# Performance work log

Measured on AMD Instinct MI355X. Metric: run time of the kernel, lower is better.

The kernel has to match this reference:

```python
import jax, jax.numpy as jnp
import numpy as np

B, S, D, H = 4, 2048, 256, 8
DH = D // H  # d_head = 32


def setup_inputs() -> dict:
    key = jax.random.key(0)
    ks = jax.random.split(key, 7)
    scale = 1.0 / np.sqrt(D)  # ~ torch Linear init range
    sequences = jax.random.normal(ks[0], (B, S, D), dtype=jnp.float32)
    Wq = jax.random.uniform(ks[1], (H, D, DH), jnp.float32, -scale, scale)
    Wk = jax.random.uniform(ks[2], (H, D, DH), jnp.float32, -scale, scale)
    Wv = jax.random.uniform(ks[3], (H, D, DH), jnp.float32, -scale, scale)
    bq = jax.random.uniform(ks[4], (H, DH), jnp.float32, -scale, scale)
    bk = jax.random.uniform(ks[5], (H, DH), jnp.float32, -scale, scale)
    bv = jax.random.uniform(ks[6], (H, DH), jnp.float32, -scale, scale)
    return {"sequences": sequences, "Wq": Wq, "Wk": Wk, "Wv": Wv,
            "bq": bq, "bk": bk, "bv": bv}


def reference(sequences, Wq, Wk, Wv, bq, bk, bv):
    # Per-head linear maps of the FULL token (use_linear_mapping=True):
    # q[b,h,s,e] = sequences[b,s,:] @ Wq[h] + bq[h]
    q = jnp.einsum('bsd,hde->bhse', sequences, Wq) + bq[None, :, None, :]
    k = jnp.einsum('bsd,hde->bhse', sequences, Wk) + bk[None, :, None, :]
    v = jnp.einsum('bsd,hde->bhse', sequences, Wv) + bv[None, :, None, :]
    # Scaled dot-product attention per batch/head (full SxS matrix, as original)
    scores = jnp.einsum('bhse,bhte->bhst', q, k) / jnp.sqrt(jnp.float32(DH))
    attn = jax.nn.softmax(scores, axis=-1)
    out = jnp.einsum('bhst,bhte->bhse', attn, v)
    # hstack heads along feature dim -> [B, S, D]
    return out.transpose(0, 2, 1, 3).reshape(B, S, D)
```

## Files before the change

### kernel.cpp

```cpp
#include <hip/hip_runtime.h>
#include <hip/hip_bf16.h>


#define NB 4
#define NS 2048
#define ND 256
#define NH 8
#define NDH 32
#define KT 128
#define NT (NS / KT)

typedef __attribute__((ext_vector_type(8))) short short8;
typedef __attribute__((ext_vector_type(4))) float float4v;

static __device__ __forceinline__ unsigned short f2bf(float f) {
    union { float f; unsigned int u; } v; v.f = f;
    unsigned int r = (v.u + 0x7FFFu + ((v.u >> 16) & 1u)) >> 16;
    return (unsigned short)r;
}

static __device__ __forceinline__ unsigned int pk2bf(float lo, float hi) {
    __hip_bfloat162 h = __float22bfloat162_rn(float2{lo, hi});
    union { __hip_bfloat162 h; unsigned int u; } c; c.h = h;
    return c.u;
}

#if defined(__has_builtin)
#if __has_builtin(__builtin_amdgcn_exp2f)
#define EXP2F(x) __builtin_amdgcn_exp2f(x)
#endif
#endif
#ifndef EXP2F
#define EXP2F(x) exp2f(x)
#endif

#define SWZ(x) ((x) ^ ((((x) >> 7) & 7) << 4))

__global__ __launch_bounds__(256) void prep_seq(const float* __restrict__ seq,
                                                unsigned short* __restrict__ seqb) {
    int i = (blockIdx.x * 256 + threadIdx.x) * 4;
    float4 v = *(const float4*)(seq + i);
    ushort4 o;
    o.x = f2bf(v.x); o.y = f2bf(v.y); o.z = f2bf(v.z); o.w = f2bf(v.w);
    *(ushort4*)(seqb + i) = o;
}

__global__ __launch_bounds__(256) void prep_w(const float* __restrict__ Wq,
                                              const float* __restrict__ Wk,
                                              const float* __restrict__ Wv,
                                              unsigned short* __restrict__ Wt) {
    int idx = blockIdx.x * 256 + threadIdx.x;
    int c = idx >> 8, d = idx & 255;
    int mat = c >> 8;
    int cm = c & 255;
    int h = cm >> 5, e = cm & 31;
    const float* W = (mat == 0) ? Wq : (mat == 1) ? Wk : Wv;
    Wt[c * 256 + d] = f2bf(W[(h * 256 + d) * 32 + e]);
}

__global__ __launch_bounds__(256, 2) void proj(const unsigned short* __restrict__ seqb,
                                               const unsigned short* __restrict__ Wt,
                                               const float* __restrict__ bq,
                                               const float* __restrict__ bk,
                                               const float* __restrict__ bv,
                                               unsigned short* __restrict__ Q,
                                               unsigned short* __restrict__ K,
                                               unsigned short* __restrict__ Vt) {
    __shared__ __align__(16) unsigned short plds[32768];

    int m0 = blockIdx.x * 64;
    int c0 = blockIdx.y * 64;
    int tid = (int)threadIdx.x;
    int wave = tid >> 6, lane = tid & 63;
    int g = lane >> 4, r4 = lane & 15;

#pragma unroll
    for (int j = 0; j < 16; ++j) {
        int s = tid + 256 * j;
        int local = s & 2047;
        int row = local >> 5;
        int col16 = (local & 31) ^ (row & 7);
        const unsigned short* src = (s < 2048)
            ? (seqb + (size_t)(m0 + row) * 256 + col16 * 8)
            : (Wt + (size_t)(c0 + row) * 256 + col16 * 8);
        __builtin_amdgcn_global_load_lds(
            (const __attribute__((address_space(1))) unsigned int*)src,
            (__attribute__((address_space(3))) unsigned int*)(&plds[s * 8]), 16, 0, 0);
    }
    __syncthreads();

    const unsigned short* ldsA = plds;
    const unsigned short* ldsB = plds + 16384;
    int rowA = wave * 16 + r4;
    int xA = r4 & 7;

    float4v acc[4];
#pragma unroll
    for (int ct = 0; ct < 4; ++ct) acc[ct] = (float4v){0.f, 0.f, 0.f, 0.f};

#pragma unroll
    for (int i = 0; i < 8; ++i) {
        int cp = ((4 * i + g) ^ xA) * 8;
        short8 a = *(const short8*)(ldsA + rowA * 256 + cp);
#pragma unroll
        for (int ct = 0; ct < 4; ++ct) {
            short8 b = *(const short8*)(ldsB + (ct * 16 + r4) * 256 + cp);
            acc[ct] = __builtin_amdgcn_mfma_f32_16x16x32_bf16(a, b, acc[ct], 0, 0, 0);
        }
    }

    const float SC = 0.17677669529663687f * 1.4426950408889634f;
#pragma unroll
    for (int ct = 0; ct < 4; ++ct) {
        int c = c0 + ct * 16 + r4;
        int mat = c >> 8;
        int cm = c & 255;
        int h = cm >> 5, e = cm & 31;
        float bias = ((mat == 0) ? bq : (mat == 1) ? bk : bv)[cm];
#pragma unroll
        for (int r = 0; r < 4; ++r) {
            int m = m0 + wave * 16 + 4 * g + r;
            int b = m >> 11, s = m & 2047;
            float val = acc[ct][r] + bias;
            if (mat == 0) {
                Q[((b * NH + h) * NS + s) * NDH + e] = f2bf(val * SC);
            } else if (mat == 1) {
                K[((b * NH + h) * NS + s) * NDH + e] = f2bf(val);
            } else {
                Vt[((b * NH + h) * NDH + e) * NS + s] = f2bf(val);
            }
        }
    }
}

__global__ __launch_bounds__(256, 2) void attn_kernel(const unsigned short* __restrict__ Q,
                                                      const unsigned short* __restrict__ K,
                                                      const unsigned short* __restrict__ Vt,
                                                      float* __restrict__ out) {
    __shared__ __align__(16) unsigned short lds[2][8192];

    int bx = (int)blockIdx.x;
    int wid = (bx & 7) * 64 + (bx >> 3);
    int bh = wid >> 4;
    int qt = wid & 15;
    int tid = (int)threadIdx.x;
    int wave = tid >> 6, lane = tid & 63;
    int g = lane >> 4, r4 = lane & 15;
    int q0 = qt * 128 + wave * 32;

    const unsigned short* Qb = Q + (size_t)bh * NS * NDH;
    const unsigned short* Kb = K + (size_t)bh * NS * NDH;
    const unsigned short* Vb = Vt + (size_t)bh * NDH * NS;

    const unsigned short* sgp;
    int strideT;
    int strideB;
    unsigned int sloff;
    {
        int slot = tid & 127;
        int sL = slot ^ ((slot >> 3) & 7);
        int row = sL >> 2, c16 = sL & 3;
        if (tid < 128) {
            int key = (row < 16) ? (2 * row) : (2 * (row - 16) + 1);
            sgp = Kb + key * NDH + c16 * 8;
            strideT = KT * NDH;
            strideB = 32 * NDH;
            sloff = slot * 8;
        } else {
            sgp = Vb + row * NS + c16 * 8;
            strideT = KT;
            strideB = 32;
            sloff = 1024 + slot * 8;
        }
    }

#define STAGE(bufi, t)                                                                        \
    do {                                                                                      \
        const unsigned short* _s = sgp + (size_t)(t) * strideT;                               \
        __builtin_amdgcn_global_load_lds(                                                     \
            (const __attribute__((address_space(1))) unsigned int*)(_s),                      \
            (__attribute__((address_space(3))) unsigned int*)(&lds[bufi][sloff]), 16, 0, 0);  \
        __builtin_amdgcn_global_load_lds(                                                     \
            (const __attribute__((address_space(1))) unsigned int*)(_s + strideB),            \
            (__attribute__((address_space(3))) unsigned int*)(&lds[bufi][sloff + 2048]), 16, 0, 0); \
        __builtin_amdgcn_global_load_lds(                                                     \
            (const __attribute__((address_space(1))) unsigned int*)(_s + 2 * strideB),        \
            (__attribute__((address_space(3))) unsigned int*)(&lds[bufi][sloff + 4096]), 16, 0, 0); \
        __builtin_amdgcn_global_load_lds(                                                     \
            (const __attribute__((address_space(1))) unsigned int*)(_s + 3 * strideB),        \
            (__attribute__((address_space(3))) unsigned int*)(&lds[bufi][sloff + 6144]), 16, 0, 0); \
    } while (0)

    int kOff0 = SWZ(r4 * 64 + g * 16);
    int kOff1 = SWZ((16 + r4) * 64 + g * 16);
    int vOff0 = 2048 + SWZ(r4 * 64 + g * 16);
    int vOff1 = 2048 + SWZ((16 + r4) * 64 + g * 16);

    short8 qf0 = *(const short8*)(Qb + (q0 + r4) * NDH + 8 * g);
    short8 qf1 = *(const short8*)(Qb + (q0 + 16 + r4) * NDH + 8 * g);

    float4v accA0 = {0.f, 0.f, 0.f, 0.f}, accB0 = {0.f, 0.f, 0.f, 0.f};
    float4v accA1 = {0.f, 0.f, 0.f, 0.f}, accB1 = {0.f, 0.f, 0.f, 0.f};
    const float4v zero = {0.f, 0.f, 0.f, 0.f};
    float l0 = 0.f, l1 = 0.f;

    auto process = [&](const char* buf) {
        short8 kf0 = *(const short8*)(buf + kOff0);
        short8 kf1 = *(const short8*)(buf + kOff1);
        short8 va0 = *(const short8*)(buf + vOff0);
        short8 va1 = *(const short8*)(buf + vOff1);
        {
            float4v s0 = __builtin_amdgcn_mfma_f32_16x16x32_bf16(kf0, qf0, zero, 0, 0, 0);
            float4v s1 = __builtin_amdgcn_mfma_f32_16x16x32_bf16(kf1, qf0, zero, 0, 0, 0);
            union { short8 s; unsigned int u[4]; } pb;
#pragma unroll
            for (int r = 0; r < 4; ++r) {
                float pe = EXP2F(s0[r]), po = EXP2F(s1[r]);
                l0 += pe + po;
                pb.u[r] = pk2bf(pe, po);
            }
            accA0 = __builtin_amdgcn_mfma_f32_16x16x32_bf16(va0, pb.s, accA0, 0, 0, 0);
            accB0 = __builtin_amdgcn_mfma_f32_16x16x32_bf16(va1, pb.s, accB0, 0, 0, 0);
        }
        {
            float4v s0 = __builtin_amdgcn_mfma_f32_16x16x32_bf16(kf0, qf1, zero, 0, 0, 0);
            float4v s1 = __builtin_amdgcn_mfma_f32_16x16x32_bf16(kf1, qf1, zero, 0, 0, 0);
            union { short8 s; unsigned int u[4]; } pb;
#pragma unroll
            for (int r = 0; r < 4; ++r) {
                float pe = EXP2F(s0[r]), po = EXP2F(s1[r]);
                l1 += pe + po;
                pb.u[r] = pk2bf(pe, po);
            }
            accA1 = __builtin_amdgcn_mfma_f32_16x16x32_bf16(va0, pb.s, accA1, 0, 0, 0);
            accB1 = __builtin_amdgcn_mfma_f32_16x16x32_bf16(va1, pb.s, accB1, 0, 0, 0);
        }
    };

    STAGE(0, 0);

    int cur = 0;
    for (int t = 0; t < NT; ++t) {
        if (t + 1 < NT) {
            STAGE(cur ^ 1, t + 1);
            asm volatile("s_waitcnt vmcnt(4)" ::: "memory");
        } else {
            asm volatile("s_waitcnt vmcnt(0)" ::: "memory");
        }
        __builtin_amdgcn_sched_barrier(0);
        __builtin_amdgcn_s_barrier();

        __builtin_amdgcn_s_setprio(1);
        const char* buf = (const char*)lds[cur];
        process(buf);
        process(buf + 4096);
        process(buf + 8192);
        process(buf + 12288);
        __builtin_amdgcn_s_setprio(0);

        __builtin_amdgcn_sched_barrier(0);
        __builtin_amdgcn_s_barrier();
        cur ^= 1;
    }

    l0 += __shfl_xor(l0, 16); l0 += __shfl_xor(l0, 32);
    l1 += __shfl_xor(l1, 16); l1 += __shfl_xor(l1, 32);
    float linv0 = 1.0f / l0, linv1 = 1.0f / l1;

    int b = bh >> 3, h = bh & 7;
    {
        int s = q0 + r4;
        float* op = out + (size_t)(b * NS + s) * ND + h * NDH;
        float4 oa = {accA0[0] * linv0, accA0[1] * linv0, accA0[2] * linv0, accA0[3] * linv0};
        float4 ob = {accB0[0] * linv0, accB0[1] * linv0, accB0[2] * linv0, accB0[3] * linv0};
        *(float4*)(op + 4 * g) = oa;
        *(float4*)(op + 16 + 4 * g) = ob;
    }
    {
        int s = q0 + 16 + r4;
        float* op = out + (size_t)(b * NS + s) * ND + h * NDH;
        float4 oa = {accA1[0] * linv1, accA1[1] * linv1, accA1[2] * linv1, accA1[3] * linv1};
        float4 ob = {accB1[0] * linv1, accB1[1] * linv1, accB1[2] * linv1, accB1[3] * linv1};
        *(float4*)(op + 4 * g) = oa;
        *(float4*)(op + 16 + 4 * g) = ob;
    }
#undef STAGE
}

extern "C" void kernel_launch(void* const* d_in, const int* in_sizes, int n_in,
                              void* d_out, int out_size, void* d_ws, size_t ws_size,
                              hipStream_t stream) {
    const float* seq = (const float*)d_in[0];
    const float* Wq = (const float*)d_in[1];
    const float* Wk = (const float*)d_in[2];
    const float* Wv = (const float*)d_in[3];
    const float* bq = (const float*)d_in[4];
    const float* bk = (const float*)d_in[5];
    const float* bv = (const float*)d_in[6];
    float* out = (float*)d_out;

    unsigned short* seqb = (unsigned short*)d_ws;
    unsigned short* Wt = seqb + 2097152;
    unsigned short* Qw = Wt + 196608;
    unsigned short* Kw = Qw + 2097152;
    unsigned short* Vtw = Kw + 2097152;

    hipLaunchKernelGGL(prep_seq, dim3(2048), dim3(256), 0, stream, seq, seqb);
    hipLaunchKernelGGL(prep_w, dim3(768), dim3(256), 0, stream, Wq, Wk, Wv, Wt);
    hipLaunchKernelGGL(proj, dim3(128, 12), dim3(256), 0, stream, seqb, Wt, bq, bk, bv, Qw, Kw, Vtw);
    hipLaunchKernelGGL(attn_kernel, dim3(512), dim3(256), 0, stream, Qw, Kw, Vtw, out);
}
```

Baseline: 61.72 us.

## Triple-buffer attention K/V loads, compute row sums via MFMA, merge prep kernels

The attention loop moves from double to triple buffering in LDS. It prefetches two tiles ahead and uses a single barrier per iteration, which should hide global load latency better. The softmax denominator is now accumulated with an extra MFMA against a ones vector instead of scalar adds and cross-lane shuffles, and accumulators are split into even and odd sets to shorten MFMA dependency chains. The two prep kernels are fused into one launch; the costs are more LDS per block, more accumulator registers, and the row sum being computed from bf16-rounded probabilities.

```diff
diff --git a/kernel.cpp b/kernel.cpp
--- a/kernel.cpp
+++ b/kernel.cpp
@@ -36,26 +36,28 @@
 
 #define SWZ(x) ((x) ^ ((((x) >> 7) & 7) << 4))
 
-__global__ __launch_bounds__(256) void prep_seq(const float* __restrict__ seq,
-                                                unsigned short* __restrict__ seqb) {
-    int i = (blockIdx.x * 256 + threadIdx.x) * 4;
-    float4 v = *(const float4*)(seq + i);
-    ushort4 o;
-    o.x = f2bf(v.x); o.y = f2bf(v.y); o.z = f2bf(v.z); o.w = f2bf(v.w);
-    *(ushort4*)(seqb + i) = o;
-}
-
-__global__ __launch_bounds__(256) void prep_w(const float* __restrict__ Wq,
-                                              const float* __restrict__ Wk,
-                                              const float* __restrict__ Wv,
-                                              unsigned short* __restrict__ Wt) {
-    int idx = blockIdx.x * 256 + threadIdx.x;
-    int c = idx >> 8, d = idx & 255;
-    int mat = c >> 8;
-    int cm = c & 255;
-    int h = cm >> 5, e = cm & 31;
-    const float* W = (mat == 0) ? Wq : (mat == 1) ? Wk : Wv;
-    Wt[c * 256 + d] = f2bf(W[(h * 256 + d) * 32 + e]);
+__global__ __launch_bounds__(256) void prep(const float* __restrict__ seq,
+                                            unsigned short* __restrict__ seqb,
+                                            const float* __restrict__ Wq,
+                                            const float* __restrict__ Wk,
+                                            const float* __restrict__ Wv,
+                                            unsigned short* __restrict__ Wt) {
+    int bx = (int)blockIdx.x;
+    if (bx < 2048) {
+        int i = (bx * 256 + (int)threadIdx.x) * 4;
+        float4 v = *(const float4*)(seq + i);
+        ushort4 o;
+        o.x = f2bf(v.x); o.y = f2bf(v.y); o.z = f2bf(v.z); o.w = f2bf(v.w);
+        *(ushort4*)(seqb + i) = o;
+    } else {
+        int idx = (bx - 2048) * 256 + (int)threadIdx.x;
+        int c = idx >> 8, d = idx & 255;
+        int mat = c >> 8;
+        int cm = c & 255;
+        int h = cm >> 5, e = cm & 31;
+        const float* W = (mat == 0) ? Wq : (mat == 1) ? Wk : Wv;
+        Wt[c * 256 + d] = f2bf(W[(h * 256 + d) * 32 + e]);
+    }
 }
 
 __global__ __launch_bounds__(256, 2) void proj(const unsigned short* __restrict__ seqb,
@@ -137,7 +139,7 @@
                                                       const unsigned short* __restrict__ K,
                                                       const unsigned short* __restrict__ Vt,
                                                       float* __restrict__ out) {
-    __shared__ __align__(16) unsigned short lds[2][8192];
+    __shared__ __align__(16) unsigned short lds[3][8192];
 
     int bx = (int)blockIdx.x;
     int wid = (bx & 7) * 64 + (bx >> 3);
@@ -199,12 +201,16 @@
     short8 qf0 = *(const short8*)(Qb + (q0 + r4) * NDH + 8 * g);
     short8 qf1 = *(const short8*)(Qb + (q0 + 16 + r4) * NDH + 8 * g);
 
-    float4v accA0 = {0.f, 0.f, 0.f, 0.f}, accB0 = {0.f, 0.f, 0.f, 0.f};
-    float4v accA1 = {0.f, 0.f, 0.f, 0.f}, accB1 = {0.f, 0.f, 0.f, 0.f};
+    const short ONE = (short)0x3F80;
+    const short8 ones = {ONE, ONE, ONE, ONE, ONE, ONE, ONE, ONE};
+
+    float4v aA0e = {0,0,0,0}, aB0e = {0,0,0,0}, aA1e = {0,0,0,0}, aB1e = {0,0,0,0};
+    float4v aA0o = {0,0,0,0}, aB0o = {0,0,0,0}, aA1o = {0,0,0,0}, aB1o = {0,0,0,0};
+    float4v lc0e = {0,0,0,0}, lc1e = {0,0,0,0}, lc0o = {0,0,0,0}, lc1o = {0,0,0,0};
     const float4v zero = {0.f, 0.f, 0.f, 0.f};
-    float l0 = 0.f, l1 = 0.f;
-
-    auto process = [&](const char* buf) {
+
+    auto process = [&](const char* buf, float4v& A0, float4v& B0, float4v& L0,
+                       float4v& A1, float4v& B1, float4v& L1) {
         short8 kf0 = *(const short8*)(buf + kOff0);
         short8 kf1 = *(const short8*)(buf + kOff1);
         short8 va0 = *(const short8*)(buf + vOff0);
@@ -214,58 +220,58 @@
             float4v s1 = __builtin_amdgcn_mfma_f32_16x16x32_bf16(kf1, qf0, zero, 0, 0, 0);
             union { short8 s; unsigned int u[4]; } pb;
 #pragma unroll
-            for (int r = 0; r < 4; ++r) {
-                float pe = EXP2F(s0[r]), po = EXP2F(s1[r]);
-                l0 += pe + po;
-                pb.u[r] = pk2bf(pe, po);
-            }
-            accA0 = __builtin_amdgcn_mfma_f32_16x16x32_bf16(va0, pb.s, accA0, 0, 0, 0);
-            accB0 = __builtin_amdgcn_mfma_f32_16x16x32_bf16(va1, pb.s, accB0, 0, 0, 0);
+            for (int r = 0; r < 4; ++r)
+                pb.u[r] = pk2bf(EXP2F(s0[r]), EXP2F(s1[r]));
+            A0 = __builtin_amdgcn_mfma_f32_16x16x32_bf16(va0, pb.s, A0, 0, 0, 0);
+            B0 = __builtin_amdgcn_mfma_f32_16x16x32_bf16(va1, pb.s, B0, 0, 0, 0);
+            L0 = __builtin_amdgcn_mfma_f32_16x16x32_bf16(ones, pb.s, L0, 0, 0, 0);
         }
         {
             float4v s0 = __builtin_amdgcn_mfma_f32_16x16x32_bf16(kf0, qf1, zero, 0, 0, 0);
             float4v s1 = __builtin_amdgcn_mfma_f32_16x16x32_bf16(kf1, qf1, zero, 0, 0, 0);
             union { short8 s; unsigned int u[4]; } pb;
 #pragma unroll
-            for (int r = 0; r < 4; ++r) {
-                float pe = EXP2F(s0[r]), po = EXP2F(s1[r]);
-                l1 += pe + po;
-                pb.u[r] = pk2bf(pe, po);
-            }
-            accA1 = __builtin_amdgcn_mfma_f32_16x16x32_bf16(va0, pb.s, accA1, 0, 0, 0);
-            accB1 = __builtin_amdgcn_mfma_f32_16x16x32_bf16(va1, pb.s, accB1, 0, 0, 0);
+            for (int r = 0; r < 4; ++r)
+                pb.u[r] = pk2bf(EXP2F(s0[r]), EXP2F(s1[r]));
+            A1 = __builtin_amdgcn_mfma_f32_16x16x32_bf16(va0, pb.s, A1, 0, 0, 0);
+            B1 = __builtin_amdgcn_mfma_f32_16x16x32_bf16(va1, pb.s, B1, 0, 0, 0);
+            L1 = __builtin_amdgcn_mfma_f32_16x16x32_bf16(ones, pb.s, L1, 0, 0, 0);
         }
     };
 
     STAGE(0, 0);
+    STAGE(1, 1);
 
     int cur = 0;
     for (int t = 0; t < NT; ++t) {
-        if (t + 1 < NT) {
-            STAGE(cur ^ 1, t + 1);
+        __builtin_amdgcn_s_barrier();
+        if (t + 2 < NT) {
+            int fut = cur + 2; if (fut >= 3) fut -= 3;
+            STAGE(fut, t + 2);
+            asm volatile("s_waitcnt vmcnt(8)" ::: "memory");
+        } else if (t + 1 < NT) {
             asm volatile("s_waitcnt vmcnt(4)" ::: "memory");
         } else {
             asm volatile("s_waitcnt vmcnt(0)" ::: "memory");
         }
         __builtin_amdgcn_sched_barrier(0);
-        __builtin_amdgcn_s_barrier();
 
         __builtin_amdgcn_s_setprio(1);
         const char* buf = (const char*)lds[cur];
-        process(buf);
-        process(buf + 4096);
-        process(buf + 8192);
-        process(buf + 12288);
+        process(buf,         aA0e, aB0e, lc0e, aA1e, aB1e, lc1e);
+        process(buf + 4096,  aA0o, aB0o, lc0o, aA1o, aB1o, lc1o);
+        process(buf + 8192,  aA0e, aB0e, lc0e, aA1e, aB1e, lc1e);
+        process(buf + 12288, aA0o, aB0o, lc0o, aA1o, aB1o, lc1o);
         __builtin_amdgcn_s_setprio(0);
 
         __builtin_amdgcn_sched_barrier(0);
-        __builtin_amdgcn_s_barrier();
-        cur ^= 1;
-    }
-
-    l0 += __shfl_xor(l0, 16); l0 += __shfl_xor(l0, 32);
-    l1 += __shfl_xor(l1, 16); l1 += __shfl_xor(l1, 32);
-    float linv0 = 1.0f / l0, linv1 = 1.0f / l1;
+        ++cur; if (cur >= 3) cur -= 3;
+    }
+
+    float4v accA0 = aA0e + aA0o, accB0 = aB0e + aB0o;
+    float4v accA1 = aA1e + aA1o, accB1 = aB1e + aB1o;
+    float linv0 = 1.0f / (lc0e[0] + lc0o[0]);
+    float linv1 = 1.0f / (lc1e[0] + lc1o[0]);
 
     int b = bh >> 3, h = bh & 7;
     {
@@ -305,8 +311,7 @@
     unsigned short* Kw = Qw + 2097152;
     unsigned short* Vtw = Kw + 2097152;
 
-    hipLaunchKernelGGL(prep_seq, dim3(2048), dim3(256), 0, stream, seq, seqb);
-    hipLaunchKernelGGL(prep_w, dim3(768), dim3(256), 0, stream, Wq, Wk, Wv, Wt);
+    hipLaunchKernelGGL(prep, dim3(2816), dim3(256), 0, stream, seq, seqb, Wq, Wk, Wv, Wt);
     hipLaunchKernelGGL(proj, dim3(128, 12), dim3(256), 0, stream, seqb, Wt, bq, bk, bv, Qw, Kw, Vtw);
     hipLaunchKernelGGL(attn_kernel, dim3(512), dim3(256), 0, stream, Qw, Kw, Vtw, out);
 }
```

Result: faster. 57.05 us (-7.6%).
